# Optimization experiments

Hardware: AMD Instinct MI355X
Metric: run time of the kernel (lower is better)

## Reference

```python
import jax, jax.numpy as jnp
import numpy as np

NUM_HEADS = 4
WINDOW = 7
DILATION = 1
NEG_MIN = jnp.finfo(jnp.float32).min


def _offsets():
    r = WINDOW // 2
    return [(i - r) * DILATION for i in range(WINDOW)]


def _gather_neighbors(x):
    # x: [B, C, H, W] -> [B, C, K, H, W] with zero padding outside bounds.
    B, C, H, W = x.shape
    offs = _offsets()
    r = (WINDOW // 2) * DILATION
    xp = jnp.pad(x, ((0, 0), (0, 0), (r, r), (r, r)))
    slices = [xp[:, :, r + dy:r + dy + H, r + dx:r + dx + W]
              for dy in offs for dx in offs]
    return jnp.stack(slices, axis=2)


def _valid_mask(H, W):
    # [K, H, W] bool: neighbor (h+dy, w+dx) is inside the image.
    offs = _offsets()
    hh = jnp.arange(H)[:, None]
    ww = jnp.arange(W)[None, :]
    masks = [((hh + dy >= 0) & (hh + dy < H) & (ww + dx >= 0) & (ww + dx < W))
             for dy in offs for dx in offs]
    return jnp.stack(masks, axis=0)


def setup_inputs() -> dict:
    key = jax.random.key(0)
    k1, k2, k3 = jax.random.split(key, 3)
    shape = (2, 64, 96, 96)
    return {
        "q": jax.random.normal(k1, shape, dtype=jnp.float32),
        "k": jax.random.normal(k2, shape, dtype=jnp.float32),
        "v": jax.random.normal(k3, shape, dtype=jnp.float32),
    }


def reference(q, k, v):
    B, C, H, W = q.shape
    d_head = C // NUM_HEADS
    K = WINDOW * WINDOW

    q_heads = q.reshape(B, NUM_HEADS, d_head, H, W)
    k_nb = _gather_neighbors(k).reshape(B, NUM_HEADS, d_head, K, H, W)
    v_nb = _gather_neighbors(v).reshape(B, NUM_HEADS, d_head, K, H, W)
    # [B, heads, K, d_head, H, W]
    k_nb = jnp.transpose(k_nb, (0, 1, 3, 2, 4, 5))
    v_nb = jnp.transpose(v_nb, (0, 1, 3, 2, 4, 5))

    scale = 1.0 / jnp.sqrt(jnp.float32(d_head))
    scores = jnp.einsum('bhdyx,bhkdyx->bhkyx', q_heads, k_nb) * scale
    mask = _valid_mask(H, W)[None, None]  # [1,1,K,H,W]
    scores = jnp.where(mask, scores, NEG_MIN)
    attn = jax.nn.softmax(scores, axis=2)
    out = jnp.einsum('bhkyx,bhkdyx->bhdyx', attn, v_nb)
    return out.reshape(B, C, H, W)
```

## Files before the change

### kernel.cpp

```cpp
#include <hip/hip_runtime.h>

#define HH 96
#define WW 96
#define CH 64
#define NHEADS 4
#define DHEAD 16
#define BATCH 2
#define PLANE (HH * WW)

#define BROWS 6
#define BCOLS 16
#define HROWS (BROWS + 6)
#define HCOLS (BCOLS + 6)
#define KPITCH 20
#define KPIX (HROWS * HCOLS)
#define KPIXA (KPIX + 10)
#define VPITCH 24
#define VCH (HROWS * VPITCH + 8)
#define TY_N (HH / BROWS)
#define TX_N (WW / BCOLS)

typedef _Float16 half4 __attribute__((ext_vector_type(4)));
typedef float f32x4 __attribute__((ext_vector_type(4)));
typedef _Float16 h2 __attribute__((ext_vector_type(2)));
union H2U { unsigned int u; h2 h; };

template <bool INTERIOR>
__device__ __forceinline__ void block_body(
    const float* __restrict__ q, const float* __restrict__ k,
    const float* __restrict__ v, float* __restrict__ out,
    _Float16* __restrict__ lk, _Float16* __restrict__ lv,
    int c0, int h0, int w0)
{
    const int tid = threadIdx.x;

    const int lane = tid & 63;
    const int wid  = tid >> 6;
    const int lp   = lane & 15;
    const int lg   = lane >> 4;
    const int h    = h0 + wid;

    const float QS = 0.25f * 1.4426950408889634f;
    const int qbase = (c0 + lg * 4) * PLANE + h * WW + w0 + lp;
    half4 qf;
    qf.x = (_Float16)(q[qbase] * QS);
    qf.y = (_Float16)(q[qbase + PLANE] * QS);
    qf.z = (_Float16)(q[qbase + 2 * PLANE] * QS);
    qf.w = (_Float16)(q[qbase + 3 * PLANE] * QS);

    {
        const int col = tid & 31;
        const int sp0 = tid >> 5;
#pragma unroll 2
        for (int r = 0; r < 8; ++r) {
            const int sid = r * 12 + sp0;
            const int row = sid >> 3;
            const int cp  = sid & 7;
            if (col < HCOLS) {
                int gh = h0 - 3 + row;
                int gw = w0 - 3 + col;
                if constexpr (!INTERIOR) {
                    gh = min(max(gh, 0), HH - 1);
                    gw = min(max(gw, 0), WW - 1);
                }
                const float* p0 = k + (size_t)(c0 + cp * 2) * PLANE + gh * WW + gw;
                H2U t;
                t.h.x = (_Float16)p0[0];
                t.h.y = (_Float16)p0[PLANE];
                *(h2*)&lk[(row * HCOLS + col) * KPITCH + cp * 2] = t.h;
            }
        }
    }

    {
        const int l16  = tid & 15;
        const int sq0  = tid >> 4;
        const int col0 = l16 * 2;
#pragma unroll 2
        for (int r = 0; r < 8; ++r) {
            const int sid = r * 24 + sq0;
            const int row = sid >> 4;
            const int ch  = sid & 15;
            if (col0 <= HCOLS) {
                H2U t;
                if (col0 < HCOLS) {
                    int gh = h0 - 3 + row;
                    int ga = w0 - 3 + col0;
                    int gb = ga + 1;
                    if constexpr (!INTERIOR) {
                        gh = min(max(gh, 0), HH - 1);
                        ga = min(max(ga, 0), WW - 1);
                        gb = min(max(gb, 0), WW - 1);
                    }
                    const float* p0 = v + (size_t)(c0 + ch) * PLANE + gh * WW;
                    t.h.x = (_Float16)p0[ga];
                    t.h.y = (_Float16)p0[gb];
                } else {
                    t.u = 0;
                }
                *(h2*)&lv[ch * VCH + row * VPITCH + col0] = t.h;
            }
        }
    }

    {
        H2U z; z.u = 0;
        if (tid < 100)
            *(h2*)&lk[KPIX * KPITCH + tid * 2] = z.h;
        if (tid < 64)
            *(h2*)&lv[(tid >> 2) * VCH + 288 + (tid & 3) * 2] = z.h;
    }
    __syncthreads();

    bool ok1[4], ok2[4];
#pragma unroll
    for (int e = 0; e < 4; ++e) {
        const int j1 = lg * 4 + e;
        const int j2 = 16 + j1;
        ok1[e] = ((unsigned)(j1 - lp) < 7u);
        ok2[e] = ((unsigned)(j2 - lp) < 7u);
        if constexpr (!INTERIOR) {
            ok1[e] = ok1[e] && ((unsigned)(w0 - 3 + j1) < (unsigned)WW);
            ok2[e] = ok2[e] && ((unsigned)(w0 - 3 + j2) < (unsigned)WW);
        }
    }

    f32x4 acc = {0.f, 0.f, 0.f, 0.f};
    float ssA = 0.f, ssB = 0.f;

#pragma unroll
    for (int dy = 0; dy < 7; ++dy) {
        if constexpr (!INTERIOR) {
            if ((unsigned)(h + dy - 3) >= (unsigned)HH) continue;
        }
        const int r = wid + dy;

        const half4 ka1 = *(const half4*)&lk[(r * HCOLS + lp) * KPITCH + lg * 4];
        const half4 ka2 = *(const half4*)&lk[(r * HCOLS + 16 + lp) * KPITCH + lg * 4];
        const f32x4 zz = {0.f, 0.f, 0.f, 0.f};
        f32x4 s1 = __builtin_amdgcn_mfma_f32_16x16x16f16(ka1, qf, zz, 0, 0, 0);
        f32x4 s2 = __builtin_amdgcn_mfma_f32_16x16x16f16(ka2, qf, zz, 0, 0, 0);

        half4 p1, p2;
#pragma unroll
        for (int e = 0; e < 4; ++e) {
            const float e1 = ok1[e] ? __builtin_amdgcn_exp2f(s1[e]) : 0.f;
            const float e2 = ok2[e] ? __builtin_amdgcn_exp2f(s2[e]) : 0.f;
            ssA += e1;
            ssB += e2;
            p1[e] = (_Float16)e1;
            p2[e] = (_Float16)e2;
        }

        const half4 va1 = *(const half4*)&lv[lp * VCH + r * VPITCH + lg * 4];
        const half4 va2 = *(const half4*)&lv[lp * VCH + r * VPITCH + 16 + lg * 4];
        acc = __builtin_amdgcn_mfma_f32_16x16x16f16(va1, p1, acc, 0, 0, 0);
        acc = __builtin_amdgcn_mfma_f32_16x16x16f16(va2, p2, acc, 0, 0, 0);
    }

    float ssum = ssA + ssB;
    ssum += __shfl_xor(ssum, 16, 64);
    ssum += __shfl_xor(ssum, 32, 64);
    const float inv = 1.0f / ssum;

    const int obase = (c0 + lg * 4) * PLANE + h * WW + w0 + lp;
#pragma unroll
    for (int e = 0; e < 4; ++e)
        out[obase + e * PLANE] = acc[e] * inv;
}

__global__ __launch_bounds__(384)
__attribute__((amdgpu_waves_per_eu(8)))
void natten_mfma6(
    const float* __restrict__ q, const float* __restrict__ k,
    const float* __restrict__ v, float* __restrict__ out)
{
    __shared__ __align__(16) _Float16 lk[KPIXA * KPITCH];
    __shared__ __align__(16) _Float16 lv[16 * VCH];

    const int bid  = (int)blockIdx.x;
    const int slab = bid & 7;
    const int t    = bid >> 3;
    const int b = slab >> 2, head = slab & 3;
    const int ty = t / TX_N, tx = t % TX_N;
    const int c0 = b * CH + head * DHEAD;
    const int h0 = ty * BROWS, w0 = tx * BCOLS;

    const bool interior = (ty >= 1) && (ty <= TY_N - 2) &&
                          (tx >= 1) && (tx <= TX_N - 2);
    if (interior)
        block_body<true >(q, k, v, out, lk, lv, c0, h0, w0);
    else
        block_body<false>(q, k, v, out, lk, lv, c0, h0, w0);
}

extern "C" void kernel_launch(void* const* d_in, const int* in_sizes, int n_in,
                              void* d_out, int out_size, void* d_ws, size_t ws_size,
                              hipStream_t stream) {
    const float* q = (const float*)d_in[0];
    const float* k = (const float*)d_in[1];
    const float* v = (const float*)d_in[2];
    float* out = (float*)d_out;

    const int grid = BATCH * NHEADS * TY_N * TX_N;
    natten_mfma6<<<grid, 384, 0, stream>>>(q, k, v, out);
}
```

Before: 15.47 us.

## Align halo to even columns and load K/V tiles with float2 vector loads

Widens the shared-memory halo to 24 columns starting one column further left, so interior blocks can fetch K and V with aligned float2 global loads, batched into registers before converting and storing to LDS. The window validity masks are shifted by one to match the new halo origin. The change also packs softmax probabilities with cvt_pkrtz, splits the PV accumulator in two to break the MFMA dependency chain, and lowers the waves-per-EU hint from 8 to 5. The trade-off is more registers held for the batched loads, lower occupancy, a slightly larger LDS tile, and strided 2-byte LDS stores for K.

```diff
diff --git a/kernel.cpp b/kernel.cpp
--- a/kernel.cpp
+++ b/kernel.cpp
@@ -11,19 +11,31 @@
 #define BROWS 6
 #define BCOLS 16
 #define HROWS (BROWS + 6)
-#define HCOLS (BCOLS + 6)
+#define HCOLS 24
 #define KPITCH 20
 #define KPIX (HROWS * HCOLS)
-#define KPIXA (KPIX + 10)
-#define VPITCH 24
+#define KPIXA (KPIX + 8)
+#define VPITCH HCOLS
 #define VCH (HROWS * VPITCH + 8)
 #define TY_N (HH / BROWS)
 #define TX_N (WW / BCOLS)
 
 typedef _Float16 half4 __attribute__((ext_vector_type(4)));
+typedef _Float16 h2 __attribute__((ext_vector_type(2)));
 typedef float f32x4 __attribute__((ext_vector_type(4)));
-typedef _Float16 h2 __attribute__((ext_vector_type(2)));
-union H2U { unsigned int u; h2 h; };
+
+__device__ __forceinline__ half4 pack4(float a, float b, float c, float d) {
+#if __has_builtin(__builtin_amdgcn_cvt_pkrtz)
+    h2 lo = __builtin_bit_cast(h2, __builtin_amdgcn_cvt_pkrtz(a, b));
+    h2 hi = __builtin_bit_cast(h2, __builtin_amdgcn_cvt_pkrtz(c, d));
+    half4 r; r.x = lo.x; r.y = lo.y; r.z = hi.x; r.w = hi.y;
+    return r;
+#else
+    half4 r; r.x = (_Float16)a; r.y = (_Float16)b;
+    r.z = (_Float16)c; r.w = (_Float16)d;
+    return r;
+#endif
+}
 
 template <bool INTERIOR>
 __device__ __forceinline__ void block_body(
@@ -48,67 +60,85 @@
     qf.z = (_Float16)(q[qbase + 2 * PLANE] * QS);
     qf.w = (_Float16)(q[qbase + 3 * PLANE] * QS);
 
+    const int l16  = tid & 15;
+    const int grp  = tid >> 4;
+    const int col0 = l16 * 2;
+    const bool act = (col0 < HCOLS);
+
+    if constexpr (INTERIOR) {
+        float2 kb[8];
+#pragma unroll
+        for (int r = 0; r < 8; ++r) {
+            const int sid = r * 24 + grp;
+            const int row = sid >> 4, ch = sid & 15;
+            if (act)
+                kb[r] = *(const float2*)(k + (size_t)(c0 + ch) * PLANE +
+                                         (h0 - 3 + row) * WW + (w0 - 4) + col0);
+        }
+#pragma unroll
+        for (int r = 0; r < 8; ++r) {
+            const int sid = r * 24 + grp;
+            const int row = sid >> 4, ch = sid & 15;
+            if (act) {
+                const int pix = row * HCOLS + col0;
+                lk[pix * KPITCH + ch]       = (_Float16)kb[r].x;
+                lk[(pix + 1) * KPITCH + ch] = (_Float16)kb[r].y;
+            }
+        }
+        float2 vb[8];
+#pragma unroll
+        for (int r = 0; r < 8; ++r) {
+            const int sid = r * 24 + grp;
+            const int row = sid >> 4, ch = sid & 15;
+            if (act)
+                vb[r] = *(const float2*)(v + (size_t)(c0 + ch) * PLANE +
+                                         (h0 - 3 + row) * WW + (w0 - 4) + col0);
+        }
+#pragma unroll
+        for (int r = 0; r < 8; ++r) {
+            const int sid = r * 24 + grp;
+            const int row = sid >> 4, ch = sid & 15;
+            if (act) {
+                h2 t; t.x = (_Float16)vb[r].x; t.y = (_Float16)vb[r].y;
+                *(h2*)&lv[ch * VCH + row * VPITCH + col0] = t;
+            }
+        }
+    } else {
+#pragma unroll
+        for (int r = 0; r < 8; ++r) {
+            const int sid = r * 24 + grp;
+            const int row = sid >> 4, ch = sid & 15;
+            if (act) {
+                const int gh = min(max(h0 - 3 + row, 0), HH - 1);
+                const int ga = min(max(w0 - 4 + col0, 0), WW - 1);
+                const int gb = min(max(w0 - 3 + col0, 0), WW - 1);
+                const float* p0 = k + (size_t)(c0 + ch) * PLANE + gh * WW;
+                const int pix = row * HCOLS + col0;
+                lk[pix * KPITCH + ch]       = (_Float16)p0[ga];
+                lk[(pix + 1) * KPITCH + ch] = (_Float16)p0[gb];
+            }
+        }
+#pragma unroll
+        for (int r = 0; r < 8; ++r) {
+            const int sid = r * 24 + grp;
+            const int row = sid >> 4, ch = sid & 15;
+            if (act) {
+                const int gh = min(max(h0 - 3 + row, 0), HH - 1);
+                const int ga = min(max(w0 - 4 + col0, 0), WW - 1);
+                const int gb = min(max(w0 - 3 + col0, 0), WW - 1);
+                const float* p0 = v + (size_t)(c0 + ch) * PLANE + gh * WW;
+                h2 t; t.x = (_Float16)p0[ga]; t.y = (_Float16)p0[gb];
+                *(h2*)&lv[ch * VCH + row * VPITCH + col0] = t;
+            }
+        }
+    }
+
     {
-        const int col = tid & 31;
-        const int sp0 = tid >> 5;
-#pragma unroll 2
-        for (int r = 0; r < 8; ++r) {
-            const int sid = r * 12 + sp0;
-            const int row = sid >> 3;
-            const int cp  = sid & 7;
-            if (col < HCOLS) {
-                int gh = h0 - 3 + row;
-                int gw = w0 - 3 + col;
-                if constexpr (!INTERIOR) {
-                    gh = min(max(gh, 0), HH - 1);
-                    gw = min(max(gw, 0), WW - 1);
-                }
-                const float* p0 = k + (size_t)(c0 + cp * 2) * PLANE + gh * WW + gw;
-                H2U t;
-                t.h.x = (_Float16)p0[0];
-                t.h.y = (_Float16)p0[PLANE];
-                *(h2*)&lk[(row * HCOLS + col) * KPITCH + cp * 2] = t.h;
-            }
-        }
-    }
-
-    {
-        const int l16  = tid & 15;
-        const int sq0  = tid >> 4;
-        const int col0 = l16 * 2;
-#pragma unroll 2
-        for (int r = 0; r < 8; ++r) {
-            const int sid = r * 24 + sq0;
-            const int row = sid >> 4;
-            const int ch  = sid & 15;
-            if (col0 <= HCOLS) {
-                H2U t;
-                if (col0 < HCOLS) {
-                    int gh = h0 - 3 + row;
-                    int ga = w0 - 3 + col0;
-                    int gb = ga + 1;
-                    if constexpr (!INTERIOR) {
-                        gh = min(max(gh, 0), HH - 1);
-                        ga = min(max(ga, 0), WW - 1);
-                        gb = min(max(gb, 0), WW - 1);
-                    }
-                    const float* p0 = v + (size_t)(c0 + ch) * PLANE + gh * WW;
-                    t.h.x = (_Float16)p0[ga];
-                    t.h.y = (_Float16)p0[gb];
-                } else {
-                    t.u = 0;
-                }
-                *(h2*)&lv[ch * VCH + row * VPITCH + col0] = t.h;
-            }
-        }
-    }
-
-    {
-        H2U z; z.u = 0;
-        if (tid < 100)
-            *(h2*)&lk[KPIX * KPITCH + tid * 2] = z.h;
+        h2 z; z.x = (_Float16)0.f; z.y = (_Float16)0.f;
+        if (tid < 80)
+            *(h2*)&lk[KPIX * KPITCH + tid * 2] = z;
         if (tid < 64)
-            *(h2*)&lv[(tid >> 2) * VCH + 288 + (tid & 3) * 2] = z.h;
+            *(h2*)&lv[(tid >> 2) * VCH + HROWS * VPITCH + (tid & 3) * 2] = z;
     }
     __syncthreads();
 
@@ -117,15 +147,16 @@
     for (int e = 0; e < 4; ++e) {
         const int j1 = lg * 4 + e;
         const int j2 = 16 + j1;
-        ok1[e] = ((unsigned)(j1 - lp) < 7u);
-        ok2[e] = ((unsigned)(j2 - lp) < 7u);
+        ok1[e] = ((unsigned)(j1 - lp - 1) < 7u);
+        ok2[e] = ((unsigned)(j2 - lp - 1) < 7u);
         if constexpr (!INTERIOR) {
-            ok1[e] = ok1[e] && ((unsigned)(w0 - 3 + j1) < (unsigned)WW);
-            ok2[e] = ok2[e] && ((unsigned)(w0 - 3 + j2) < (unsigned)WW);
-        }
-    }
-
-    f32x4 acc = {0.f, 0.f, 0.f, 0.f};
+            ok1[e] = ok1[e] && ((unsigned)(w0 - 4 + j1) < (unsigned)WW);
+            ok2[e] = ok2[e] && ((unsigned)(w0 - 4 + j2) < (unsigned)WW);
+        }
+    }
+
+    f32x4 accA = {0.f, 0.f, 0.f, 0.f};
+    f32x4 accB = {0.f, 0.f, 0.f, 0.f};
     float ssA = 0.f, ssB = 0.f;
 
 #pragma unroll
@@ -141,21 +172,23 @@
         f32x4 s1 = __builtin_amdgcn_mfma_f32_16x16x16f16(ka1, qf, zz, 0, 0, 0);
         f32x4 s2 = __builtin_amdgcn_mfma_f32_16x16x16f16(ka2, qf, zz, 0, 0, 0);
 
-        half4 p1, p2;
-#pragma unroll
-        for (int e = 0; e < 4; ++e) {
-            const float e1 = ok1[e] ? __builtin_amdgcn_exp2f(s1[e]) : 0.f;
-            const float e2 = ok2[e] ? __builtin_amdgcn_exp2f(s2[e]) : 0.f;
-            ssA += e1;
-            ssB += e2;
-            p1[e] = (_Float16)e1;
-            p2[e] = (_Float16)e2;
-        }
+        const float e10 = ok1[0] ? __builtin_amdgcn_exp2f(s1[0]) : 0.f;
+        const float e11 = ok1[1] ? __builtin_amdgcn_exp2f(s1[1]) : 0.f;
+        const float e12 = ok1[2] ? __builtin_amdgcn_exp2f(s1[2]) : 0.f;
+        const float e13 = ok1[3] ? __builtin_amdgcn_exp2f(s1[3]) : 0.f;
+        const float e20 = ok2[0] ? __builtin_amdgcn_exp2f(s2[0]) : 0.f;
+        const float e21 = ok2[1] ? __builtin_amdgcn_exp2f(s2[1]) : 0.f;
+        const float e22 = ok2[2] ? __builtin_amdgcn_exp2f(s2[2]) : 0.f;
+        const float e23 = ok2[3] ? __builtin_amdgcn_exp2f(s2[3]) : 0.f;
+        ssA += (e10 + e11) + (e12 + e13);
+        ssB += (e20 + e21) + (e22 + e23);
+        const half4 p1 = pack4(e10, e11, e12, e13);
+        const half4 p2 = pack4(e20, e21, e22, e23);
 
         const half4 va1 = *(const half4*)&lv[lp * VCH + r * VPITCH + lg * 4];
         const half4 va2 = *(const half4*)&lv[lp * VCH + r * VPITCH + 16 + lg * 4];
-        acc = __builtin_amdgcn_mfma_f32_16x16x16f16(va1, p1, acc, 0, 0, 0);
-        acc = __builtin_amdgcn_mfma_f32_16x16x16f16(va2, p2, acc, 0, 0, 0);
+        accA = __builtin_amdgcn_mfma_f32_16x16x16f16(va1, p1, accA, 0, 0, 0);
+        accB = __builtin_amdgcn_mfma_f32_16x16x16f16(va2, p2, accB, 0, 0, 0);
     }
 
     float ssum = ssA + ssB;
@@ -163,6 +196,8 @@
     ssum += __shfl_xor(ssum, 32, 64);
     const float inv = 1.0f / ssum;
 
+    const f32x4 acc = accA + accB;
+
     const int obase = (c0 + lg * 4) * PLANE + h * WW + w0 + lp;
 #pragma unroll
     for (int e = 0; e < 4; ++e)
@@ -170,8 +205,8 @@
 }
 
 __global__ __launch_bounds__(384)
-__attribute__((amdgpu_waves_per_eu(8)))
-void natten_mfma6(
+__attribute__((amdgpu_waves_per_eu(5)))
+void natten_mfma6b(
     const float* __restrict__ q, const float* __restrict__ k,
     const float* __restrict__ v, float* __restrict__ out)
 {
@@ -203,5 +238,5 @@
     float* out = (float*)d_out;
 
     const int grid = BATCH * NHEADS * TY_N * TX_N;
-    natten_mfma6<<<grid, 384, 0, stream>>>(q, k, v, out);
-}
+    natten_mfma6b<<<grid, 384, 0, stream>>>(q, k, v, out);
+}
```

After: 14.93 us (median of 3 runs). 3.5% less time.
